# Optimization experiments

Measured on AMD Instinct MI355X. Metric: run time of the kernel, lower is better.

Reference implementation:

```python
import jax, jax.numpy as jnp
import numpy as np

N_NODES = 100000
N_EDGES = 1200000
IN_FEATS = 30
HIDDEN = 64


def setup_inputs() -> dict:
    key = jax.random.key(0)
    k = jax.random.split(key, 6)
    x = jax.random.normal(k[0], (N_NODES, IN_FEATS), dtype=jnp.float32)
    W1 = jax.random.normal(k[1], (IN_FEATS, HIDDEN), dtype=jnp.float32) * (1.0 / np.sqrt(IN_FEATS))
    b1 = jnp.zeros((HIDDEN,), dtype=jnp.float32)
    W2 = jax.random.normal(k[2], (HIDDEN, HIDDEN), dtype=jnp.float32) * (1.0 / np.sqrt(HIDDEN))
    b2 = jnp.zeros((HIDDEN,), dtype=jnp.float32)
    src = jax.random.randint(k[3], (N_EDGES,), 0, N_NODES, dtype=jnp.int32)
    dst = jax.random.randint(k[4], (N_EDGES,), 0, N_NODES, dtype=jnp.int32)
    return {"x": x, "W1": W1, "b1": b1, "W2": W2, "b2": b2, "src": src, "dst": dst}


def _graph_conv(h, W, b, src, dst, norm_src, norm_dst, n_nodes):
    # DGL GraphConv, norm='both': D_in^{-1/2} A D_out^{-1/2} h W + b, then relu
    h = h * norm_src[:, None]          # [N, din] scale by out-degree^{-1/2}
    h = h @ W                          # [N, dout] dense transform
    agg = jax.ops.segment_sum(h[src], dst, num_segments=n_nodes)  # sparse aggregation
    return jax.nn.relu(agg * norm_dst[:, None] + b)


def reference(x, W1, b1, W2, b2, src, dst):
    n = x.shape[0]
    ones = jnp.ones(src.shape, dtype=x.dtype)
    out_deg = jax.ops.segment_sum(ones, src, num_segments=n)
    in_deg = jax.ops.segment_sum(ones, dst, num_segments=n)
    norm_src = jnp.maximum(out_deg, 1.0) ** -0.5
    norm_dst = jnp.maximum(in_deg, 1.0) ** -0.5
    h = _graph_conv(x, W1, b1, src, dst, norm_src, norm_dst, n)
    h = _graph_conv(h, W2, b2, src, dst, norm_src, norm_dst, n)
    return h
```

## Files before the change

### kernel.cpp

```cpp
#include <hip/hip_runtime.h>
#include <hip/hip_fp16.h>

constexpr int IN_FEATS = 30;
constexpr int HIDDEN   = 64;
constexpr int SCAN_CHUNK = 1024;
constexpr int RB_BITS = 9;
constexpr int RB_MASK = (1 << RB_BITS) - 1;
constexpr int ECHUNK  = 2048;
constexpr int NPB     = 32;

__global__ __launch_bounds__(256) void part_count(
    const int* __restrict__ src, const int* __restrict__ dst,
    int* __restrict__ cntT, int nE, int NBK, int NCH, int NK2)
{
    __shared__ int binsD[256], binsS[256];
    int b = blockIdx.x, t = threadIdx.x;
    binsD[t] = 0; binsS[t] = 0;
    __syncthreads();
    int base = b * ECHUNK;
#pragma unroll
    for (int i = 0; i < ECHUNK / 256; ++i) {
        int e = base + t + i * 256;
        if (e < nE) {
            atomicAdd(&binsD[dst[e] >> RB_BITS], 1);
            atomicAdd(&binsS[src[e] >> RB_BITS], 1);
        }
    }
    __syncthreads();
    if (t < NBK) {
        cntT[t * NCH + b]       = binsD[t];
        cntT[NK2 + t * NCH + b] = binsS[t];
    }
}

__global__ __launch_bounds__(256) void scan_partial(
    const int* __restrict__ deg, int* __restrict__ blockSum, int n)
{
    __shared__ int part[256];
    int b = blockIdx.x, t = threadIdx.x;
    int base = b * SCAN_CHUNK + t * 4;
    int s = 0;
#pragma unroll
    for (int j = 0; j < 4; ++j) { int i = base + j; if (i < n) s += deg[i]; }
    part[t] = s;
    __syncthreads();
    for (int off = 1; off < 256; off <<= 1) {
        int add = (t >= off) ? part[t - off] : 0;
        __syncthreads();
        part[t] += add;
        __syncthreads();
    }
    if (t == 255) blockSum[b] = part[255];
}

__global__ __launch_bounds__(1024) void scan_offsets(int* blockSum, int nB, int* totalPtr)
{
    __shared__ int part[1024];
    int t = threadIdx.x;
    int v = (t < nB) ? blockSum[t] : 0;
    part[t] = v;
    __syncthreads();
    for (int off = 1; off < 1024; off <<= 1) {
        int add = (t >= off) ? part[t - off] : 0;
        __syncthreads();
        part[t] += add;
        __syncthreads();
    }
    if (t < nB) blockSum[t] = part[t] - v;
    if (totalPtr && t == nB - 1) *totalPtr = part[t];
}

__global__ __launch_bounds__(256) void scan_final(
    const int* __restrict__ deg, const int* __restrict__ blockSum,
    int* __restrict__ outp, int n)
{
    __shared__ int part[256];
    int b = blockIdx.x, t = threadIdx.x;
    int base = b * SCAN_CHUNK + t * 4;
    int v[4];
    int s = 0;
#pragma unroll
    for (int j = 0; j < 4; ++j) { int i = base + j; v[j] = (i < n) ? deg[i] : 0; s += v[j]; }
    part[t] = s;
    __syncthreads();
    for (int off = 1; off < 256; off <<= 1) {
        int add = (t >= off) ? part[t - off] : 0;
        __syncthreads();
        part[t] += add;
        __syncthreads();
    }
    int run = blockSum[b] + part[t] - s;
#pragma unroll
    for (int j = 0; j < 4; ++j) {
        int i = base + j;
        if (i < n) outp[i] = run;
        run += v[j];
    }
}

__global__ __launch_bounds__(256) void part_scatter(
    const int* __restrict__ src, const int* __restrict__ dst,
    const int* __restrict__ ofsT, unsigned int* __restrict__ pairs,
    unsigned short* __restrict__ sloc, int nE, int NBK, int NCH, int NK2)
{
    __shared__ int bins[256], lstart[256], lcur[256], gofs[256], part[256], scur[256];
    __shared__ int lsrc[ECHUNK], ldst[ECHUNK];
    int b = blockIdx.x, t = threadIdx.x;
    bins[t] = 0;
    if (t < NBK) {
        gofs[t] = ofsT[t * NCH + b];
        scur[t] = ofsT[NK2 + t * NCH + b] - nE;
    }
    __syncthreads();
    int base = b * ECHUNK;
    int rs[ECHUNK / 256], rd[ECHUNK / 256];
#pragma unroll
    for (int i = 0; i < ECHUNK / 256; ++i) {
        int e = base + t + i * 256;
        rs[i] = -1;
        if (e < nE) {
            rs[i] = src[e]; rd[i] = dst[e];
            atomicAdd(&bins[rd[i] >> RB_BITS], 1);
        }
    }
#pragma unroll
    for (int i = 0; i < ECHUNK / 256; ++i) {
        if (rs[i] >= 0) {
            int s = rs[i];
            int pos = atomicAdd(&scur[s >> RB_BITS], 1);
            sloc[pos] = (unsigned short)(s & RB_MASK);
        }
    }
    __syncthreads();
    int v = bins[t];
    part[t] = v;
    __syncthreads();
    for (int off = 1; off < 256; off <<= 1) {
        int add = (t >= off) ? part[t - off] : 0;
        __syncthreads();
        part[t] += add;
        __syncthreads();
    }
    lstart[t] = part[t] - v;
    lcur[t]   = part[t] - v;
    __syncthreads();
#pragma unroll
    for (int i = 0; i < ECHUNK / 256; ++i) {
        if (rs[i] >= 0) {
            int k = rd[i] >> RB_BITS;
            int p = atomicAdd(&lcur[k], 1);
            lsrc[p] = rs[i]; ldst[p] = rd[i];
        }
    }
    __syncthreads();
    int cE = min(ECHUNK, nE - base);
    for (int j = t; j < cE; j += 256) {
        int d = ldst[j], k = d >> RB_BITS;
        int g = gofs[k] + (j - lstart[k]);
        pairs[g] = ((unsigned int)(d & RB_MASK) << 23) | (unsigned int)lsrc[j];
    }
}

__global__ __launch_bounds__(256) void bucket_build(
    const unsigned int* __restrict__ pairs, const int* __restrict__ ofsT,
    int* __restrict__ degI, int* __restrict__ rowptr, int* __restrict__ csr,
    int nE, int n, int NBK, int NCH)
{
    __shared__ int bins[512];
    __shared__ int part[256];
    __shared__ int cur[512];
    int k = blockIdx.x, t = threadIdx.x;
    bins[t] = 0; bins[t + 256] = 0;
    __syncthreads();
    int begin = ofsT[k * NCH];
    int end   = (k + 1 < NBK) ? ofsT[(k + 1) * NCH] : nE;
    for (int e = begin + t; e < end; e += 256)
        atomicAdd(&bins[pairs[e] >> 23], 1);
    __syncthreads();
    int v0 = bins[2 * t], v1 = bins[2 * t + 1];
    int s = v0 + v1;
    part[t] = s;
    __syncthreads();
    for (int off = 1; off < 256; off <<= 1) {
        int add = (t >= off) ? part[t - off] : 0;
        __syncthreads();
        part[t] += add;
        __syncthreads();
    }
    int pre = part[t] - s;
    int base = k << RB_BITS;
    int n0 = base + 2 * t, n1 = n0 + 1;
    int r0 = begin + pre, r1 = r0 + v0;
    cur[2 * t] = r0; cur[2 * t + 1] = r1;
    if (n0 < n) { degI[n0] = v0; rowptr[n0] = r0; }
    if (n1 < n) { degI[n1] = v1; rowptr[n1] = r1; }
    if (k == NBK - 1 && t == 0) rowptr[n] = nE;
    __syncthreads();
    for (int e = begin + t; e < end; e += 256) {
        unsigned int u = pairs[e];
        int p = atomicAdd(&cur[u >> 23], 1);
        csr[p] = (int)(u & 0x7FFFFFu);
    }
}

__global__ __launch_bounds__(256) void bucket_srcside(
    const unsigned short* __restrict__ sloc, const int* __restrict__ ofsT,
    const float* __restrict__ x, int* __restrict__ degO,
    unsigned int* __restrict__ xn, int nE, int n, int NBK, int NCH, int NK2)
{
    __shared__ int bins[512];
    int k = blockIdx.x, t = threadIdx.x;
    bins[t] = 0; bins[t + 256] = 0;
    __syncthreads();
    int begin = ofsT[NK2 + k * NCH] - nE;
    int end   = (k + 1 < NBK) ? (ofsT[NK2 + (k + 1) * NCH] - nE) : nE;
    for (int e = begin + t; e < end; e += 256)
        atomicAdd(&bins[sloc[e]], 1);
    __syncthreads();
    int base = k << RB_BITS;
    if (base + t < n)       degO[base + t]       = bins[t];
    if (base + 256 + t < n) degO[base + 256 + t] = bins[t + 256];
#pragma unroll 4
    for (int i = 0; i < 32; ++i) {
        int idx = t + 256 * i;
        int nl = idx >> 4, p = idx & 15;
        int node = base + nl;
        if (node < n) {
            float ns = rsqrtf(fmaxf((float)bins[nl], 1.0f));
            float a = (2 * p     < IN_FEATS) ? x[(size_t)node * IN_FEATS + 2 * p]     * ns : 0.0f;
            float b = (2 * p + 1 < IN_FEATS) ? x[(size_t)node * IN_FEATS + 2 * p + 1] * ns : 0.0f;
            __half2 h = __floats2half2_rn(a, b);
            xn[(size_t)node * 16 + p] = *reinterpret_cast<unsigned int*>(&h);
        }
    }
}

__global__ __launch_bounds__(256) void gather_x2(
    const unsigned int* __restrict__ xn, const int* __restrict__ csr,
    const int* __restrict__ rowptr, float* __restrict__ aggx, int n)
{
    int wv   = (blockIdx.x * 256 + threadIdx.x) >> 6;
    int lane = threadIdx.x & 63;
    if (wv >= n) return;
    int begin = rowptr[wv], end = rowptr[wv + 1];
    int g = lane >> 2;
    int p = lane & 3;
    float a0 = 0, a1 = 0, a2 = 0, a3 = 0, a4 = 0, a5 = 0, a6 = 0, a7 = 0;
    int e = begin + g;
    for (; e + 16 < end; e += 32) {
        int s0 = csr[e], s1 = csr[e + 16];
        uint4 u0 = *reinterpret_cast<const uint4*>(xn + (size_t)s0 * 16 + 4 * p);
        uint4 u1 = *reinterpret_cast<const uint4*>(xn + (size_t)s1 * 16 + 4 * p);
        float2 v;
        v = __half22float2(*reinterpret_cast<__half2*>(&u0.x)); a0 += v.x; a1 += v.y;
        v = __half22float2(*reinterpret_cast<__half2*>(&u0.y)); a2 += v.x; a3 += v.y;
        v = __half22float2(*reinterpret_cast<__half2*>(&u0.z)); a4 += v.x; a5 += v.y;
        v = __half22float2(*reinterpret_cast<__half2*>(&u0.w)); a6 += v.x; a7 += v.y;
        v = __half22float2(*reinterpret_cast<__half2*>(&u1.x)); a0 += v.x; a1 += v.y;
        v = __half22float2(*reinterpret_cast<__half2*>(&u1.y)); a2 += v.x; a3 += v.y;
        v = __half22float2(*reinterpret_cast<__half2*>(&u1.z)); a4 += v.x; a5 += v.y;
        v = __half22float2(*reinterpret_cast<__half2*>(&u1.w)); a6 += v.x; a7 += v.y;
    }
    if (e < end) {
        int s0 = csr[e];
        uint4 u0 = *reinterpret_cast<const uint4*>(xn + (size_t)s0 * 16 + 4 * p);
        float2 v;
        v = __half22float2(*reinterpret_cast<__half2*>(&u0.x)); a0 += v.x; a1 += v.y;
        v = __half22float2(*reinterpret_cast<__half2*>(&u0.y)); a2 += v.x; a3 += v.y;
        v = __half22float2(*reinterpret_cast<__half2*>(&u0.z)); a4 += v.x; a5 += v.y;
        v = __half22float2(*reinterpret_cast<__half2*>(&u0.w)); a6 += v.x; a7 += v.y;
    }
#pragma unroll
    for (int m = 4; m <= 32; m <<= 1) {
        a0 += __shfl_xor(a0, m); a1 += __shfl_xor(a1, m);
        a2 += __shfl_xor(a2, m); a3 += __shfl_xor(a3, m);
        a4 += __shfl_xor(a4, m); a5 += __shfl_xor(a5, m);
        a6 += __shfl_xor(a6, m); a7 += __shfl_xor(a7, m);
    }
    if (g == 0) {
        *reinterpret_cast<float4*>(aggx + (size_t)wv * 32 + 8 * p)     = make_float4(a0, a1, a2, a3);
        *reinterpret_cast<float4*>(aggx + (size_t)wv * 32 + 8 * p + 4) = make_float4(a4, a5, a6, a7);
    }
}

__global__ __launch_bounds__(256) void transform1(
    const float* __restrict__ aggx, const float* __restrict__ W1,
    const float* __restrict__ b1, const int* __restrict__ degI,
    const int* __restrict__ degO, unsigned int* __restrict__ h1s, int n)
{
    __shared__ float w[32 * HIDDEN];
    __shared__ float rows[NPB][32];
    int t = threadIdx.x;
    int node0 = blockIdx.x * NPB;
    {
        const float4* w4 = (const float4*)W1;
        float4* lw4 = (float4*)w;
#pragma unroll
        for (int i = 0; i < 2; ++i) {
            int idx = t + 256 * i;
            if (idx < 480)      lw4[idx] = w4[idx];
            else if (idx < 512) lw4[idx] = make_float4(0.f, 0.f, 0.f, 0.f);
        }
    }
    {
        int node = node0 + (t >> 3);
        if (node < n)
            *reinterpret_cast<float4*>(&rows[t >> 3][(t & 7) * 4]) =
                *reinterpret_cast<const float4*>(aggx + (size_t)node * 32 + (t & 7) * 4);
    }
    __syncthreads();
    int f = t & 63, g = t >> 6;
    float acc[8] = {0, 0, 0, 0, 0, 0, 0, 0};
#pragma unroll 2
    for (int k = 0; k < 32; k += 4) {
        float w0 = w[(k + 0) * 64 + f], w1 = w[(k + 1) * 64 + f];
        float w2v = w[(k + 2) * 64 + f], w3 = w[(k + 3) * 64 + f];
#pragma unroll
        for (int j = 0; j < 8; ++j) {
            float4 rv = *reinterpret_cast<const float4*>(&rows[g * 8 + j][k]);
            acc[j] = fmaf(rv.x, w0, acc[j]);
            acc[j] = fmaf(rv.y, w1, acc[j]);
            acc[j] = fmaf(rv.z, w2v, acc[j]);
            acc[j] = fmaf(rv.w, w3, acc[j]);
        }
    }
    float bv = b1[f];
#pragma unroll
    for (int j = 0; j < 8; ++j) {
        int node = node0 + g * 8 + j;
        float hv = 0.0f;
        if (node < n) {
            float ndv = rsqrtf(fmaxf((float)degI[node], 1.0f));
            float nsv = rsqrtf(fmaxf((float)degO[node], 1.0f));
            hv = fmaxf(fmaf(acc[j], ndv, bv), 0.0f) * nsv;
        }
        float hv1 = __shfl_down(hv, 1);
        if (node < n && (f & 1) == 0) {
            __half2 h = __floats2half2_rn(hv, hv1);
            h1s[(size_t)node * 32 + (f >> 1)] = *reinterpret_cast<unsigned int*>(&h);
        }
    }
}

__global__ __launch_bounds__(256) void gather_h2(
    const unsigned int* __restrict__ h, const int* __restrict__ csr,
    const int* __restrict__ rowptr, float* __restrict__ agg, int n)
{
    int wv   = (blockIdx.x * 256 + threadIdx.x) >> 6;
    int lane = threadIdx.x & 63;
    if (wv >= n) return;
    int begin = rowptr[wv], end = rowptr[wv + 1];
    int g = lane >> 3;
    int p = lane & 7;
    float a0 = 0, a1 = 0, a2 = 0, a3 = 0, a4 = 0, a5 = 0, a6 = 0, a7 = 0;
    int e = begin + g;
    for (; e + 8 < end; e += 16) {
        int s0 = csr[e], s1 = csr[e + 8];
        uint4 u0 = *reinterpret_cast<const uint4*>(h + (size_t)s0 * 32 + 4 * p);
        uint4 u1 = *reinterpret_cast<const uint4*>(h + (size_t)s1 * 32 + 4 * p);
        float2 v;
        v = __half22float2(*reinterpret_cast<__half2*>(&u0.x)); a0 += v.x; a1 += v.y;
        v = __half22float2(*reinterpret_cast<__half2*>(&u0.y)); a2 += v.x; a3 += v.y;
        v = __half22float2(*reinterpret_cast<__half2*>(&u0.z)); a4 += v.x; a5 += v.y;
        v = __half22float2(*reinterpret_cast<__half2*>(&u0.w)); a6 += v.x; a7 += v.y;
        v = __half22float2(*reinterpret_cast<__half2*>(&u1.x)); a0 += v.x; a1 += v.y;
        v = __half22float2(*reinterpret_cast<__half2*>(&u1.y)); a2 += v.x; a3 += v.y;
        v = __half22float2(*reinterpret_cast<__half2*>(&u1.z)); a4 += v.x; a5 += v.y;
        v = __half22float2(*reinterpret_cast<__half2*>(&u1.w)); a6 += v.x; a7 += v.y;
    }
    if (e < end) {
        int s0 = csr[e];
        uint4 u0 = *reinterpret_cast<const uint4*>(h + (size_t)s0 * 32 + 4 * p);
        float2 v;
        v = __half22float2(*reinterpret_cast<__half2*>(&u0.x)); a0 += v.x; a1 += v.y;
        v = __half22float2(*reinterpret_cast<__half2*>(&u0.y)); a2 += v.x; a3 += v.y;
        v = __half22float2(*reinterpret_cast<__half2*>(&u0.z)); a4 += v.x; a5 += v.y;
        v = __half22float2(*reinterpret_cast<__half2*>(&u0.w)); a6 += v.x; a7 += v.y;
    }
#pragma unroll
    for (int m = 8; m <= 32; m <<= 1) {
        a0 += __shfl_xor(a0, m); a1 += __shfl_xor(a1, m);
        a2 += __shfl_xor(a2, m); a3 += __shfl_xor(a3, m);
        a4 += __shfl_xor(a4, m); a5 += __shfl_xor(a5, m);
        a6 += __shfl_xor(a6, m); a7 += __shfl_xor(a7, m);
    }
    if (g == 0) {
        *reinterpret_cast<float4*>(agg + (size_t)wv * 64 + 8 * p)     = make_float4(a0, a1, a2, a3);
        *reinterpret_cast<float4*>(agg + (size_t)wv * 64 + 8 * p + 4) = make_float4(a4, a5, a6, a7);
    }
}

__global__ __launch_bounds__(256) void transform2(
    float* aggout, const float* __restrict__ W2,
    const float* __restrict__ b2, const int* __restrict__ degI, int n)
{
    __shared__ float w[HIDDEN * HIDDEN];
    __shared__ float rows[NPB][HIDDEN];
    int t = threadIdx.x;
    int node0 = blockIdx.x * NPB;
    {
        const float4* w4 = (const float4*)W2;
        float4* lw4 = (float4*)w;
#pragma unroll
        for (int i = 0; i < 4; ++i) lw4[t + 256 * i] = w4[t + 256 * i];
    }
    {
#pragma unroll
        for (int i = 0; i < 2; ++i) {
            int idx = t + 256 * i;
            int node = node0 + (idx >> 4);
            if (node < n)
                *reinterpret_cast<float4*>(&rows[idx >> 4][(idx & 15) * 4]) =
                    *reinterpret_cast<const float4*>(aggout + (size_t)node * 64 + (idx & 15) * 4);
        }
    }
    __syncthreads();
    int f = t & 63, g = t >> 6;
    float acc[8] = {0, 0, 0, 0, 0, 0, 0, 0};
#pragma unroll 2
    for (int k = 0; k < 64; k += 4) {
        float w0 = w[(k + 0) * 64 + f], w1 = w[(k + 1) * 64 + f];
        float w2v = w[(k + 2) * 64 + f], w3 = w[(k + 3) * 64 + f];
#pragma unroll
        for (int j = 0; j < 8; ++j) {
            float4 rv = *reinterpret_cast<const float4*>(&rows[g * 8 + j][k]);
            acc[j] = fmaf(rv.x, w0, acc[j]);
            acc[j] = fmaf(rv.y, w1, acc[j]);
            acc[j] = fmaf(rv.z, w2v, acc[j]);
            acc[j] = fmaf(rv.w, w3, acc[j]);
        }
    }
    float bv = b2[f];
#pragma unroll
    for (int j = 0; j < 8; ++j) {
        int node = node0 + g * 8 + j;
        if (node < n) {
            float ndv = rsqrtf(fmaxf((float)degI[node], 1.0f));
            aggout[(size_t)node * 64 + f] = fmaxf(fmaf(acc[j], ndv, bv), 0.0f);
        }
    }
}

extern "C" void kernel_launch(void* const* d_in, const int* in_sizes, int n_in,
                              void* d_out, int out_size, void* d_ws, size_t ws_size,
                              hipStream_t stream)
{
    const float* x  = (const float*)d_in[0];
    const float* W1 = (const float*)d_in[1];
    const float* b1 = (const float*)d_in[2];
    const float* W2 = (const float*)d_in[3];
    const float* b2 = (const float*)d_in[4];
    const int*  src = (const int*)d_in[5];
    const int*  dst = (const int*)d_in[6];
    float* out = (float*)d_out;

    const int n  = in_sizes[0] / IN_FEATS;
    const int nE = in_sizes[5];

    const int NBK = (n + (1 << RB_BITS) - 1) >> RB_BITS;
    const int NCH = (nE + ECHUNK - 1) / ECHUNK;
    const int NK2 = NBK * NCH;

    unsigned int* pairs = (unsigned int*)d_ws;
    int* cntT = (int*)d_ws + nE;
    int* bsum = cntT + 2 * NK2;
    unsigned short* sloc = (unsigned short*)(bsum + 1024);
    unsigned int* xn  = (unsigned int*)(bsum + 1024) + (nE + 1) / 2;
    unsigned int* h1s = xn + (size_t)n * 16;
    int* degO   = (int*)(h1s + (size_t)n * 32);
    int* degI   = degO + n;
    int* rowptr = degI + n;
    int* csr    = rowptr + (n + 1);

    const int nB2 = (2 * NK2 + SCAN_CHUNK - 1) / SCAN_CHUNK;
    const int waveBlocks = (n * 64 + 255) / 256;
    const int tfBlocks   = (n + NPB - 1) / NPB;

    part_count<<<NCH, 256, 0, stream>>>(src, dst, cntT, nE, NBK, NCH, NK2);
    scan_partial<<<nB2, 256, 0, stream>>>(cntT, bsum, 2 * NK2);
    scan_offsets<<<1, 1024, 0, stream>>>(bsum, nB2, nullptr);
    scan_final<<<nB2, 256, 0, stream>>>(cntT, bsum, cntT, 2 * NK2);

    part_scatter<<<NCH, 256, 0, stream>>>(src, dst, cntT, pairs, sloc, nE, NBK, NCH, NK2);

    bucket_build<<<NBK, 256, 0, stream>>>(pairs, cntT, degI, rowptr, csr, nE, n, NBK, NCH);
    bucket_srcside<<<NBK, 256, 0, stream>>>(sloc, cntT, x, degO, xn, nE, n, NBK, NCH, NK2);

    gather_x2<<<waveBlocks, 256, 0, stream>>>(xn, csr, rowptr, out , n);
    transform1<<<tfBlocks, 256, 0, stream>>>(out, W1, b1, degI, degO, h1s, n);

    gather_h2<<<waveBlocks, 256, 0, stream>>>(h1s, csr, rowptr, out, n);
    transform2<<<tfBlocks, 256, 0, stream>>>(out, W2, b2, degI, n);
}
```

Measured before the change: 192.9 us.

## Fuse neighbor gather into dense transform kernels for both layers

Merges each layer's CSR gather kernel into its matching transform kernel. Each block gathers 32 nodes' aggregated features directly into shared memory, with one wave handling 8 nodes in sequence, and then runs the matmul. This removes the global round trip of the intermediate aggregation buffer and two kernel launches. In exchange, each wave now walks its 8 nodes serially, which lowers memory-level parallelism per wave and may reduce latency hiding for the random gathers.

```diff
diff --git a/kernel.cpp b/kernel.cpp
--- a/kernel.cpp
+++ b/kernel.cpp
@@ -7,7 +7,6 @@
 constexpr int RB_BITS = 9;
 constexpr int RB_MASK = (1 << RB_BITS) - 1;
 constexpr int ECHUNK  = 2048;
-constexpr int NPB     = 32;
 
 __global__ __launch_bounds__(256) void part_count(
     const int* __restrict__ src, const int* __restrict__ dst,
@@ -235,63 +234,16 @@
     }
 }
 
-__global__ __launch_bounds__(256) void gather_x2(
+__global__ __launch_bounds__(256) void gx_fused(
     const unsigned int* __restrict__ xn, const int* __restrict__ csr,
-    const int* __restrict__ rowptr, float* __restrict__ aggx, int n)
-{
-    int wv   = (blockIdx.x * 256 + threadIdx.x) >> 6;
-    int lane = threadIdx.x & 63;
-    if (wv >= n) return;
-    int begin = rowptr[wv], end = rowptr[wv + 1];
-    int g = lane >> 2;
-    int p = lane & 3;
-    float a0 = 0, a1 = 0, a2 = 0, a3 = 0, a4 = 0, a5 = 0, a6 = 0, a7 = 0;
-    int e = begin + g;
-    for (; e + 16 < end; e += 32) {
-        int s0 = csr[e], s1 = csr[e + 16];
-        uint4 u0 = *reinterpret_cast<const uint4*>(xn + (size_t)s0 * 16 + 4 * p);
-        uint4 u1 = *reinterpret_cast<const uint4*>(xn + (size_t)s1 * 16 + 4 * p);
-        float2 v;
-        v = __half22float2(*reinterpret_cast<__half2*>(&u0.x)); a0 += v.x; a1 += v.y;
-        v = __half22float2(*reinterpret_cast<__half2*>(&u0.y)); a2 += v.x; a3 += v.y;
-        v = __half22float2(*reinterpret_cast<__half2*>(&u0.z)); a4 += v.x; a5 += v.y;
-        v = __half22float2(*reinterpret_cast<__half2*>(&u0.w)); a6 += v.x; a7 += v.y;
-        v = __half22float2(*reinterpret_cast<__half2*>(&u1.x)); a0 += v.x; a1 += v.y;
-        v = __half22float2(*reinterpret_cast<__half2*>(&u1.y)); a2 += v.x; a3 += v.y;
-        v = __half22float2(*reinterpret_cast<__half2*>(&u1.z)); a4 += v.x; a5 += v.y;
-        v = __half22float2(*reinterpret_cast<__half2*>(&u1.w)); a6 += v.x; a7 += v.y;
-    }
-    if (e < end) {
-        int s0 = csr[e];
-        uint4 u0 = *reinterpret_cast<const uint4*>(xn + (size_t)s0 * 16 + 4 * p);
-        float2 v;
-        v = __half22float2(*reinterpret_cast<__half2*>(&u0.x)); a0 += v.x; a1 += v.y;
-        v = __half22float2(*reinterpret_cast<__half2*>(&u0.y)); a2 += v.x; a3 += v.y;
-        v = __half22float2(*reinterpret_cast<__half2*>(&u0.z)); a4 += v.x; a5 += v.y;
-        v = __half22float2(*reinterpret_cast<__half2*>(&u0.w)); a6 += v.x; a7 += v.y;
-    }
-#pragma unroll
-    for (int m = 4; m <= 32; m <<= 1) {
-        a0 += __shfl_xor(a0, m); a1 += __shfl_xor(a1, m);
-        a2 += __shfl_xor(a2, m); a3 += __shfl_xor(a3, m);
-        a4 += __shfl_xor(a4, m); a5 += __shfl_xor(a5, m);
-        a6 += __shfl_xor(a6, m); a7 += __shfl_xor(a7, m);
-    }
-    if (g == 0) {
-        *reinterpret_cast<float4*>(aggx + (size_t)wv * 32 + 8 * p)     = make_float4(a0, a1, a2, a3);
-        *reinterpret_cast<float4*>(aggx + (size_t)wv * 32 + 8 * p + 4) = make_float4(a4, a5, a6, a7);
-    }
-}
-
-__global__ __launch_bounds__(256) void transform1(
-    const float* __restrict__ aggx, const float* __restrict__ W1,
+    const int* __restrict__ rowptr, const float* __restrict__ W1,
     const float* __restrict__ b1, const int* __restrict__ degI,
     const int* __restrict__ degO, unsigned int* __restrict__ h1s, int n)
 {
     __shared__ float w[32 * HIDDEN];
-    __shared__ float rows[NPB][32];
+    __shared__ float rows[32][32];
     int t = threadIdx.x;
-    int node0 = blockIdx.x * NPB;
+    int node0 = blockIdx.x * 32;
     {
         const float4* w4 = (const float4*)W1;
         float4* lw4 = (float4*)w;
@@ -302,11 +254,51 @@
             else if (idx < 512) lw4[idx] = make_float4(0.f, 0.f, 0.f, 0.f);
         }
     }
-    {
-        int node = node0 + (t >> 3);
-        if (node < n)
-            *reinterpret_cast<float4*>(&rows[t >> 3][(t & 7) * 4]) =
-                *reinterpret_cast<const float4*>(aggx + (size_t)node * 32 + (t & 7) * 4);
+    int lane = t & 63, wid = t >> 6;
+    int gs = lane >> 2;
+    int p  = lane & 3;
+    for (int j = 0; j < 8; ++j) {
+        int slot = wid * 8 + j;
+        int node = node0 + slot;
+        if (node < n) {
+            int begin = rowptr[node], end = rowptr[node + 1];
+            float a0 = 0, a1 = 0, a2 = 0, a3 = 0, a4 = 0, a5 = 0, a6 = 0, a7 = 0;
+            int e = begin + gs;
+            for (; e + 16 < end; e += 32) {
+                int s0 = csr[e], s1 = csr[e + 16];
+                uint4 u0 = *reinterpret_cast<const uint4*>(xn + (size_t)s0 * 16 + 4 * p);
+                uint4 u1 = *reinterpret_cast<const uint4*>(xn + (size_t)s1 * 16 + 4 * p);
+                float2 v;
+                v = __half22float2(*reinterpret_cast<__half2*>(&u0.x)); a0 += v.x; a1 += v.y;
+                v = __half22float2(*reinterpret_cast<__half2*>(&u0.y)); a2 += v.x; a3 += v.y;
+                v = __half22float2(*reinterpret_cast<__half2*>(&u0.z)); a4 += v.x; a5 += v.y;
+                v = __half22float2(*reinterpret_cast<__half2*>(&u0.w)); a6 += v.x; a7 += v.y;
+                v = __half22float2(*reinterpret_cast<__half2*>(&u1.x)); a0 += v.x; a1 += v.y;
+                v = __half22float2(*reinterpret_cast<__half2*>(&u1.y)); a2 += v.x; a3 += v.y;
+                v = __half22float2(*reinterpret_cast<__half2*>(&u1.z)); a4 += v.x; a5 += v.y;
+                v = __half22float2(*reinterpret_cast<__half2*>(&u1.w)); a6 += v.x; a7 += v.y;
+            }
+            if (e < end) {
+                int s0 = csr[e];
+                uint4 u0 = *reinterpret_cast<const uint4*>(xn + (size_t)s0 * 16 + 4 * p);
+                float2 v;
+                v = __half22float2(*reinterpret_cast<__half2*>(&u0.x)); a0 += v.x; a1 += v.y;
+                v = __half22float2(*reinterpret_cast<__half2*>(&u0.y)); a2 += v.x; a3 += v.y;
+                v = __half22float2(*reinterpret_cast<__half2*>(&u0.z)); a4 += v.x; a5 += v.y;
+                v = __half22float2(*reinterpret_cast<__half2*>(&u0.w)); a6 += v.x; a7 += v.y;
+            }
+#pragma unroll
+            for (int m = 4; m <= 32; m <<= 1) {
+                a0 += __shfl_xor(a0, m); a1 += __shfl_xor(a1, m);
+                a2 += __shfl_xor(a2, m); a3 += __shfl_xor(a3, m);
+                a4 += __shfl_xor(a4, m); a5 += __shfl_xor(a5, m);
+                a6 += __shfl_xor(a6, m); a7 += __shfl_xor(a7, m);
+            }
+            if (gs == 0) {
+                *reinterpret_cast<float4*>(&rows[slot][8 * p])     = make_float4(a0, a1, a2, a3);
+                *reinterpret_cast<float4*>(&rows[slot][8 * p + 4]) = make_float4(a4, a5, a6, a7);
+            }
+        }
     }
     __syncthreads();
     int f = t & 63, g = t >> 6;
@@ -342,76 +334,66 @@
     }
 }
 
-__global__ __launch_bounds__(256) void gather_h2(
+__global__ __launch_bounds__(256) void gh_fused(
     const unsigned int* __restrict__ h, const int* __restrict__ csr,
-    const int* __restrict__ rowptr, float* __restrict__ agg, int n)
-{
-    int wv   = (blockIdx.x * 256 + threadIdx.x) >> 6;
-    int lane = threadIdx.x & 63;
-    if (wv >= n) return;
-    int begin = rowptr[wv], end = rowptr[wv + 1];
-    int g = lane >> 3;
-    int p = lane & 7;
-    float a0 = 0, a1 = 0, a2 = 0, a3 = 0, a4 = 0, a5 = 0, a6 = 0, a7 = 0;
-    int e = begin + g;
-    for (; e + 8 < end; e += 16) {
-        int s0 = csr[e], s1 = csr[e + 8];
-        uint4 u0 = *reinterpret_cast<const uint4*>(h + (size_t)s0 * 32 + 4 * p);
-        uint4 u1 = *reinterpret_cast<const uint4*>(h + (size_t)s1 * 32 + 4 * p);
-        float2 v;
-        v = __half22float2(*reinterpret_cast<__half2*>(&u0.x)); a0 += v.x; a1 += v.y;
-        v = __half22float2(*reinterpret_cast<__half2*>(&u0.y)); a2 += v.x; a3 += v.y;
-        v = __half22float2(*reinterpret_cast<__half2*>(&u0.z)); a4 += v.x; a5 += v.y;
-        v = __half22float2(*reinterpret_cast<__half2*>(&u0.w)); a6 += v.x; a7 += v.y;
-        v = __half22float2(*reinterpret_cast<__half2*>(&u1.x)); a0 += v.x; a1 += v.y;
-        v = __half22float2(*reinterpret_cast<__half2*>(&u1.y)); a2 += v.x; a3 += v.y;
-        v = __half22float2(*reinterpret_cast<__half2*>(&u1.z)); a4 += v.x; a5 += v.y;
-        v = __half22float2(*reinterpret_cast<__half2*>(&u1.w)); a6 += v.x; a7 += v.y;
-    }
-    if (e < end) {
-        int s0 = csr[e];
-        uint4 u0 = *reinterpret_cast<const uint4*>(h + (size_t)s0 * 32 + 4 * p);
-        float2 v;
-        v = __half22float2(*reinterpret_cast<__half2*>(&u0.x)); a0 += v.x; a1 += v.y;
-        v = __half22float2(*reinterpret_cast<__half2*>(&u0.y)); a2 += v.x; a3 += v.y;
-        v = __half22float2(*reinterpret_cast<__half2*>(&u0.z)); a4 += v.x; a5 += v.y;
-        v = __half22float2(*reinterpret_cast<__half2*>(&u0.w)); a6 += v.x; a7 += v.y;
-    }
-#pragma unroll
-    for (int m = 8; m <= 32; m <<= 1) {
-        a0 += __shfl_xor(a0, m); a1 += __shfl_xor(a1, m);
-        a2 += __shfl_xor(a2, m); a3 += __shfl_xor(a3, m);
-        a4 += __shfl_xor(a4, m); a5 += __shfl_xor(a5, m);
-        a6 += __shfl_xor(a6, m); a7 += __shfl_xor(a7, m);
-    }
-    if (g == 0) {
-        *reinterpret_cast<float4*>(agg + (size_t)wv * 64 + 8 * p)     = make_float4(a0, a1, a2, a3);
-        *reinterpret_cast<float4*>(agg + (size_t)wv * 64 + 8 * p + 4) = make_float4(a4, a5, a6, a7);
-    }
-}
-
-__global__ __launch_bounds__(256) void transform2(
-    float* aggout, const float* __restrict__ W2,
-    const float* __restrict__ b2, const int* __restrict__ degI, int n)
+    const int* __restrict__ rowptr, const float* __restrict__ W2,
+    const float* __restrict__ b2, const int* __restrict__ degI,
+    float* __restrict__ out, int n)
 {
     __shared__ float w[HIDDEN * HIDDEN];
-    __shared__ float rows[NPB][HIDDEN];
+    __shared__ float rows[32][HIDDEN];
     int t = threadIdx.x;
-    int node0 = blockIdx.x * NPB;
+    int node0 = blockIdx.x * 32;
     {
         const float4* w4 = (const float4*)W2;
         float4* lw4 = (float4*)w;
 #pragma unroll
         for (int i = 0; i < 4; ++i) lw4[t + 256 * i] = w4[t + 256 * i];
     }
-    {
-#pragma unroll
-        for (int i = 0; i < 2; ++i) {
-            int idx = t + 256 * i;
-            int node = node0 + (idx >> 4);
-            if (node < n)
-                *reinterpret_cast<float4*>(&rows[idx >> 4][(idx & 15) * 4]) =
-                    *reinterpret_cast<const float4*>(aggout + (size_t)node * 64 + (idx & 15) * 4);
+    int lane = t & 63, wid = t >> 6;
+    int gs = lane >> 3;
+    int p  = lane & 7;
+    for (int j = 0; j < 8; ++j) {
+        int slot = wid * 8 + j;
+        int node = node0 + slot;
+        if (node < n) {
+            int begin = rowptr[node], end = rowptr[node + 1];
+            float a0 = 0, a1 = 0, a2 = 0, a3 = 0, a4 = 0, a5 = 0, a6 = 0, a7 = 0;
+            int e = begin + gs;
+            for (; e + 8 < end; e += 16) {
+                int s0 = csr[e], s1 = csr[e + 8];
+                uint4 u0 = *reinterpret_cast<const uint4*>(h + (size_t)s0 * 32 + 4 * p);
+                uint4 u1 = *reinterpret_cast<const uint4*>(h + (size_t)s1 * 32 + 4 * p);
+                float2 v;
+                v = __half22float2(*reinterpret_cast<__half2*>(&u0.x)); a0 += v.x; a1 += v.y;
+                v = __half22float2(*reinterpret_cast<__half2*>(&u0.y)); a2 += v.x; a3 += v.y;
+                v = __half22float2(*reinterpret_cast<__half2*>(&u0.z)); a4 += v.x; a5 += v.y;
+                v = __half22float2(*reinterpret_cast<__half2*>(&u0.w)); a6 += v.x; a7 += v.y;
+                v = __half22float2(*reinterpret_cast<__half2*>(&u1.x)); a0 += v.x; a1 += v.y;
+                v = __half22float2(*reinterpret_cast<__half2*>(&u1.y)); a2 += v.x; a3 += v.y;
+                v = __half22float2(*reinterpret_cast<__half2*>(&u1.z)); a4 += v.x; a5 += v.y;
+                v = __half22float2(*reinterpret_cast<__half2*>(&u1.w)); a6 += v.x; a7 += v.y;
+            }
+            if (e < end) {
+                int s0 = csr[e];
+                uint4 u0 = *reinterpret_cast<const uint4*>(h + (size_t)s0 * 32 + 4 * p);
+                float2 v;
+                v = __half22float2(*reinterpret_cast<__half2*>(&u0.x)); a0 += v.x; a1 += v.y;
+                v = __half22float2(*reinterpret_cast<__half2*>(&u0.y)); a2 += v.x; a3 += v.y;
+                v = __half22float2(*reinterpret_cast<__half2*>(&u0.z)); a4 += v.x; a5 += v.y;
+                v = __half22float2(*reinterpret_cast<__half2*>(&u0.w)); a6 += v.x; a7 += v.y;
+            }
+#pragma unroll
+            for (int m = 8; m <= 32; m <<= 1) {
+                a0 += __shfl_xor(a0, m); a1 += __shfl_xor(a1, m);
+                a2 += __shfl_xor(a2, m); a3 += __shfl_xor(a3, m);
+                a4 += __shfl_xor(a4, m); a5 += __shfl_xor(a5, m);
+                a6 += __shfl_xor(a6, m); a7 += __shfl_xor(a7, m);
+            }
+            if (gs == 0) {
+                *reinterpret_cast<float4*>(&rows[slot][8 * p])     = make_float4(a0, a1, a2, a3);
+                *reinterpret_cast<float4*>(&rows[slot][8 * p + 4]) = make_float4(a4, a5, a6, a7);
+            }
         }
     }
     __syncthreads();
@@ -436,7 +418,7 @@
         int node = node0 + g * 8 + j;
         if (node < n) {
             float ndv = rsqrtf(fmaxf((float)degI[node], 1.0f));
-            aggout[(size_t)node * 64 + f] = fmaxf(fmaf(acc[j], ndv, bv), 0.0f);
+            out[(size_t)node * 64 + f] = fmaxf(fmaf(acc[j], ndv, bv), 0.0f);
         }
     }
 }
@@ -473,8 +455,7 @@
     int* csr    = rowptr + (n + 1);
 
     const int nB2 = (2 * NK2 + SCAN_CHUNK - 1) / SCAN_CHUNK;
-    const int waveBlocks = (n * 64 + 255) / 256;
-    const int tfBlocks   = (n + NPB - 1) / NPB;
+    const int fusedBlocks = (n + 31) / 32;
 
     part_count<<<NCH, 256, 0, stream>>>(src, dst, cntT, nE, NBK, NCH, NK2);
     scan_partial<<<nB2, 256, 0, stream>>>(cntT, bsum, 2 * NK2);
@@ -486,9 +467,7 @@
     bucket_build<<<NBK, 256, 0, stream>>>(pairs, cntT, degI, rowptr, csr, nE, n, NBK, NCH);
     bucket_srcside<<<NBK, 256, 0, stream>>>(sloc, cntT, x, degO, xn, nE, n, NBK, NCH, NK2);
 
-    gather_x2<<<waveBlocks, 256, 0, stream>>>(xn, csr, rowptr, out , n);
-    transform1<<<tfBlocks, 256, 0, stream>>>(out, W1, b1, degI, degO, h1s, n);
-
-    gather_h2<<<waveBlocks, 256, 0, stream>>>(h1s, csr, rowptr, out, n);
-    transform2<<<tfBlocks, 256, 0, stream>>>(out, W2, b2, degI, n);
-}
+    gx_fused<<<fusedBlocks, 256, 0, stream>>>(xn, csr, rowptr, W1, b1, degI, degO, h1s, n);
+
+    gh_fused<<<fusedBlocks, 256, 0, stream>>>(h1s, csr, rowptr, W2, b2, degI, out, n);
+}
```

Result: slower. 209.2 us (+8.4%).

## Scatter edge pairs directly to global buckets and double edge chunk size

Applied to the files above, without the earlier changes.

Drops the local shared-memory counting sort in part_scatter (local bin count, prefix scan, LDS staging). Each edge now takes its global bucket slot with a shared atomic and writes its packed pair straight to global memory. ECHUNK doubles so fewer blocks run and the per-block offset tables shrink. The trade is global writes that are no longer coalesced, since consecutive threads write to scattered buckets, in exchange for fewer barriers, less shared memory and less per-block overhead.

```diff
diff --git a/kernel.cpp b/kernel.cpp
--- a/kernel.cpp
+++ b/kernel.cpp
@@ -6,7 +6,7 @@
 constexpr int SCAN_CHUNK = 1024;
 constexpr int RB_BITS = 9;
 constexpr int RB_MASK = (1 << RB_BITS) - 1;
-constexpr int ECHUNK  = 2048;
+constexpr int ECHUNK  = 4096;
 constexpr int NPB     = 32;
 
 __global__ __launch_bounds__(256) void part_count(
@@ -103,61 +103,24 @@
     const int* __restrict__ ofsT, unsigned int* __restrict__ pairs,
     unsigned short* __restrict__ sloc, int nE, int NBK, int NCH, int NK2)
 {
-    __shared__ int bins[256], lstart[256], lcur[256], gofs[256], part[256], scur[256];
-    __shared__ int lsrc[ECHUNK], ldst[ECHUNK];
+    __shared__ int curD[256], curS[256];
     int b = blockIdx.x, t = threadIdx.x;
-    bins[t] = 0;
     if (t < NBK) {
-        gofs[t] = ofsT[t * NCH + b];
-        scur[t] = ofsT[NK2 + t * NCH + b] - nE;
+        curD[t] = ofsT[t * NCH + b];
+        curS[t] = ofsT[NK2 + t * NCH + b] - nE;
     }
     __syncthreads();
     int base = b * ECHUNK;
-    int rs[ECHUNK / 256], rd[ECHUNK / 256];
 #pragma unroll
     for (int i = 0; i < ECHUNK / 256; ++i) {
         int e = base + t + i * 256;
-        rs[i] = -1;
         if (e < nE) {
-            rs[i] = src[e]; rd[i] = dst[e];
-            atomicAdd(&bins[rd[i] >> RB_BITS], 1);
-        }
-    }
-#pragma unroll
-    for (int i = 0; i < ECHUNK / 256; ++i) {
-        if (rs[i] >= 0) {
-            int s = rs[i];
-            int pos = atomicAdd(&scur[s >> RB_BITS], 1);
-            sloc[pos] = (unsigned short)(s & RB_MASK);
-        }
-    }
-    __syncthreads();
-    int v = bins[t];
-    part[t] = v;
-    __syncthreads();
-    for (int off = 1; off < 256; off <<= 1) {
-        int add = (t >= off) ? part[t - off] : 0;
-        __syncthreads();
-        part[t] += add;
-        __syncthreads();
-    }
-    lstart[t] = part[t] - v;
-    lcur[t]   = part[t] - v;
-    __syncthreads();
-#pragma unroll
-    for (int i = 0; i < ECHUNK / 256; ++i) {
-        if (rs[i] >= 0) {
-            int k = rd[i] >> RB_BITS;
-            int p = atomicAdd(&lcur[k], 1);
-            lsrc[p] = rs[i]; ldst[p] = rd[i];
-        }
-    }
-    __syncthreads();
-    int cE = min(ECHUNK, nE - base);
-    for (int j = t; j < cE; j += 256) {
-        int d = ldst[j], k = d >> RB_BITS;
-        int g = gofs[k] + (j - lstart[k]);
-        pairs[g] = ((unsigned int)(d & RB_MASK) << 23) | (unsigned int)lsrc[j];
+            int s = src[e], d = dst[e];
+            int pD = atomicAdd(&curD[d >> RB_BITS], 1);
+            pairs[pD] = ((unsigned int)(d & RB_MASK) << 23) | (unsigned int)s;
+            int pS = atomicAdd(&curS[s >> RB_BITS], 1);
+            sloc[pS] = (unsigned short)(s & RB_MASK);
+        }
     }
 }
 
```

After: 201.3 us. 4.4% more time.
